# Optimization experiments

Measured on AMD Instinct MI355X. Metric: run time of the kernel, lower is better.

Reference implementation:

```python
import jax, jax.numpy as jnp
import numpy as np

# graph/batch constants
B, N_PER, DEG, FEAT, K = 64, 1024, 16, 64, 10
N = B * N_PER            # 65536 total nodes
E = N * DEG              # 1048576 edges
HID = 2 * FEAT           # 128


def setup_inputs() -> dict:
    key = jax.random.key(0)
    ks = jax.random.split(key, 10)
    x = jax.random.normal(ks[0], (N, FEAT), jnp.float32)
    # intra-graph edges: local indices in [0, n) offset by graph id * n
    offs = (jnp.arange(B, dtype=jnp.int32) * N_PER)[:, None]
    edge_src = (jax.random.randint(ks[1], (B, N_PER * DEG), 0, N_PER, jnp.int32) + offs).reshape(-1)
    edge_dst = (jax.random.randint(ks[2], (B, N_PER * DEG), 0, N_PER, jnp.int32) + offs).reshape(-1)
    uniforms = jax.random.uniform(ks[3], (N, 3 * K), jnp.float32, 1e-6, 1.0 - 1e-6)

    def lin(k, i, o):
        s = 1.0 / np.sqrt(i)
        return jax.random.uniform(k, (i, o), jnp.float32, -s, s)

    return {
        "x": x, "edge_src": edge_src, "edge_dst": edge_dst, "uniforms": uniforms,
        "W0": lin(ks[4], FEAT, HID), "b0": jnp.zeros((HID,), jnp.float32),
        "W1": lin(ks[5], HID, HID), "b1": jnp.zeros((HID,), jnp.float32),
        "Wf": lin(ks[6], HID, HID), "bf": jnp.zeros((HID,), jnp.float32),
        "W2": lin(ks[7], 2 * HID, HID), "b2": jnp.zeros((HID,), jnp.float32),
        "W3": lin(ks[8], HID, 1), "b3": jnp.zeros((1,), jnp.float32),
    }


def _gcn_norm(src, dst):
    # GCNConv: add self-loops, symmetric deg^{-1/2} normalization
    loop = jnp.arange(N, dtype=src.dtype)
    s = jnp.concatenate([src, loop])
    d = jnp.concatenate([dst, loop])
    deg = jnp.zeros((N,), jnp.float32).at[d].add(1.0)
    dinv = jax.lax.rsqrt(deg)  # deg >= 1 because of self-loops
    return s, d, dinv[s] * dinv[d]


def _gcn(h, W, b, s, d, norm):
    h = h @ W                                                   # [N, out]
    agg = jnp.zeros((N, W.shape[1]), h.dtype).at[d].add(h[s] * norm[:, None])
    return agg + b


def reference(x, edge_src, edge_dst, uniforms, W0, b0, W1, b1, Wf, bf, W2, b2, W3, b3):
    s, d, norm = _gcn_norm(edge_src, edge_dst)
    # conv0 + global max pool + fc1 -> per-graph global info
    h0 = jax.nn.relu(_gcn(x, W0, b0, s, d, norm))               # [N, HID]
    glob = jnp.max(h0.reshape(B, N_PER, HID), axis=1) @ Wf + bf  # [B, HID]
    # two applications of the SAME conv1 (as in the source)
    h = jax.nn.relu(_gcn(h0, W1, b1, s, d, norm))
    h = jax.nn.relu(_gcn(h, W1, b1, s, d, norm))
    # ConcatenateLayer: [local, tiled global] per node (dropout is eval identity)
    h = jnp.concatenate([h, jnp.repeat(glob, N_PER, axis=0)], axis=-1)  # [N, 2*HID]
    h = jax.nn.relu(_gcn(h, W2, b2, s, d, norm))
    logits = _gcn(h, W3, b3, s, d, norm).reshape(B, N_PER)      # [B, n]
    # SampleConcrete (eval): per-graph top-k threshold mask
    th = jax.lax.top_k(logits, K)[0][:, -1]                     # kth-largest per graph
    mask = (logits >= th[:, None]).astype(jnp.float32)
    return mask.reshape(N, 1)
```

## Files before the change

### kernel.cpp

```cpp
#include <hip/hip_runtime.h>
#include <math.h>

#define NB    64
#define NPER  1024
#define NTOT  65536
#define ETOT  1048576
#define FEAT  64
#define HID   128
#define KSEL  10
#define MAXDEG 64


typedef __attribute__((ext_vector_type(8))) short bf16x8;
typedef __attribute__((ext_vector_type(4))) float f32x4;

static __device__ __forceinline__ unsigned short f2bf(float x) {
    unsigned u = __float_as_uint(x);
    return (unsigned short)((u + 0x7FFFu + ((u >> 16) & 1u)) >> 16);
}
static __device__ __forceinline__ float bf2f(unsigned short s) {
    return __uint_as_float(((unsigned)s) << 16);
}

__global__ __launch_bounds__(1024) void csrpack_k(const int* __restrict__ src,
                                                  const int* __restrict__ dst,
                                                  int* __restrict__ cnt,
                                                  unsigned short* __restrict__ col16,
                                                  const float* __restrict__ W0,
                                                  const float* __restrict__ W1,
                                                  const float* __restrict__ W2,
                                                  unsigned short* __restrict__ Wph,
                                                  unsigned short* __restrict__ Wpl,
                                                  float* __restrict__ part) {
    int t = threadIdx.x;
    int b = blockIdx.x;
    if (b >= NB) {
        int pb = b - NB;
        if (pb == 40) {
            for (int i = t; i < NB * 128; i += 1024) part[i] = 0.f;
            return;
        }
        int idx = pb * 1024 + t;
        if (idx >= 320 * 128) return;
        int k = idx >> 7;
        int c = idx & 127;
        float v;
        size_t mb;
        int kk;
        if (k < 64)       { kk = k;       v = W0[kk * 128 + c]; mb = 0; }
        else if (k < 192) { kk = k - 64;  v = W1[kk * 128 + c]; mb = (size_t)64 * 128; }
        else              { kk = k - 192; v = W2[kk * 128 + c]; mb = (size_t)192 * 128; }
        unsigned short h  = f2bf(v);
        unsigned short lo = f2bf(v - bf2f(h));
        size_t d = mb + ((size_t)(kk >> 3) * 128 + c) * 8 + (kk & 7);
        Wph[d] = h;
        Wpl[d] = lo;
        return;
    }
    __shared__ int lcnt[NPER];
    int g = b;
    int gbase = g << 10;
    int ebase = g * (NPER * 16);
    lcnt[t] = 0;
    __syncthreads();
    const int* ds = dst + ebase;
    const int* ss = src + ebase;
#pragma unroll 1
    for (int i = 0; i < 16; ++i) {
        int e = i * 1024 + t;
        int d = ds[e] & (NPER - 1);
        int s = ss[e] & (NPER - 1);
        int pos = atomicAdd(&lcnt[d], 1);
        col16[(size_t)pos * NTOT + gbase + d] = (unsigned short)s;
    }
    __syncthreads();
    cnt[gbase + t] = lcnt[t];
}

__global__ __launch_bounds__(1024) void agg_k(const float* __restrict__ Z,
                                              const float* __restrict__ x,
                                              const unsigned short* __restrict__ col16,
                                              const int* __restrict__ cnt,
                                              unsigned short* __restrict__ Ah,
                                              unsigned short* __restrict__ Al,
                                              int cshift,
                                              float* __restrict__ fvec,
                                              const float* __restrict__ Wf,
                                              const float* __restrict__ bfv,
                                              const float* __restrict__ W2g,
                                              float* __restrict__ gproj,
                                              const float* __restrict__ part) {
    __shared__ float4 sy4[4096];
    int t = threadIdx.x;

    if (Wf && (int)blockIdx.x >= (int)gridDim.x - NB) {
        float* sm = (float*)sy4;
        float* mp = sm;
        float* ps = sm + 128;
        float* gl = sm + 128 + 1024;
        int gg = blockIdx.x - (gridDim.x - NB);
        int o = t & 127, s8 = t >> 7;
        if (t < 128) mp[t] = part[(size_t)gg * 128 + t];
        __syncthreads();
        float p = 0.f;
#pragma unroll
        for (int q = 0; q < 16; ++q) { int k = s8 * 16 + q; p += mp[k] * Wf[(size_t)k * 128 + o]; }
        ps[t] = p;
        __syncthreads();
        if (t < 128) {
            float a = bfv[t];
#pragma unroll
            for (int q = 0; q < 8; ++q) a += ps[q * 128 + t];
            gl[t] = a;
        }
        __syncthreads();
        p = 0.f;
#pragma unroll
        for (int q = 0; q < 16; ++q) { int k = s8 * 16 + q; p += gl[k] * W2g[(size_t)(128 + k) * 128 + o]; }
        ps[t] = p;
        __syncthreads();
        if (t < 128) {
            float a = 0.f;
#pragma unroll
            for (int q = 0; q < 8; ++q) a += ps[q * 128 + t];
            gproj[(size_t)gg * 128 + t] = a;
        }
        return;
    }

    int g = blockIdx.x >> cshift;
    int c = blockIdx.x & ((1 << cshift) - 1);
    int gbase = g << 10;

    if (x) {
#pragma unroll
        for (int j = 0; j < 4; ++j) {
            int fl = j * 1024 + t;
            int v = fl >> 2, q = fl & 3;
            float dvv = rsqrtf((float)cnt[gbase + v] + 1.0f);
            float4 z = *(const float4*)&x[(size_t)(gbase + v) * FEAT + c * 16 + q * 4];
            z.x *= dvv; z.y *= dvv; z.z *= dvv; z.w *= dvv;
            sy4[fl] = z;
        }
    } else {
        const float4* Zg4 = (const float4*)(Z + ((size_t)c * NTOT + gbase) * 16);
#pragma unroll
        for (int j = 0; j < 4; ++j) sy4[j * 1024 + t] = Zg4[j * 1024 + t];
    }
    __syncthreads();

    int f4 = t & 3;
    int vl = t >> 2;

#pragma unroll 1
    for (int pass = 0; pass < 4; ++pass) {
        int v = pass * 256 + vl;
        int gv = gbase + v;
        int n = cnt[gv];
        float dv = rsqrtf((float)n + 1.0f);
        const unsigned short* ip = col16 + gv;
        float4 acc = sy4[v * 4 + f4];
        int i = 0;
        for (; i + 4 <= n; i += 4) {
            int a0 = ip[(size_t)(i + 0) * NTOT];
            int a1 = ip[(size_t)(i + 1) * NTOT];
            int a2 = ip[(size_t)(i + 2) * NTOT];
            int a3 = ip[(size_t)(i + 3) * NTOT];
            float4 y0 = sy4[a0 * 4 + f4];
            float4 y1 = sy4[a1 * 4 + f4];
            float4 y2 = sy4[a2 * 4 + f4];
            float4 y3 = sy4[a3 * 4 + f4];
            acc.x += (y0.x + y1.x) + (y2.x + y3.x);
            acc.y += (y0.y + y1.y) + (y2.y + y3.y);
            acc.z += (y0.z + y1.z) + (y2.z + y3.z);
            acc.w += (y0.w + y1.w) + (y2.w + y3.w);
        }
        for (; i < n; ++i) {
            float4 ya = sy4[(int)ip[(size_t)i * NTOT] * 4 + f4];
            acc.x += ya.x; acc.y += ya.y; acc.z += ya.z; acc.w += ya.w;
        }
        acc.x *= dv; acc.y *= dv; acc.z *= dv; acc.w *= dv;
        int krow = c * 16 + f4 * 4;
        size_t ba = ((size_t)(krow >> 3) * NTOT + gv) * 8 + (krow & 7);
        ushort4 h, lo;
        h.x = f2bf(acc.x); lo.x = f2bf(acc.x - bf2f(h.x));
        h.y = f2bf(acc.y); lo.y = f2bf(acc.y - bf2f(h.y));
        h.z = f2bf(acc.z); lo.z = f2bf(acc.z - bf2f(h.z));
        h.w = f2bf(acc.w); lo.w = f2bf(acc.w - bf2f(h.w));
        *(ushort4*)&Ah[ba] = h;
        *(ushort4*)&Al[ba] = lo;
    }

    if (fvec && c == 0) {
        __syncthreads();
        float* sdv = (float*)sy4;
        float dv = rsqrtf((float)cnt[gbase + t] + 1.0f);
        sdv[t] = dv;
        __syncthreads();
        int n = cnt[gbase + t];
        float acc = dv;
        const unsigned short* ip = col16 + gbase + t;
        for (int i = 0; i < n; ++i) acc += sdv[ip[(size_t)i * NTOT]];
        fvec[gbase + t] = dv * acc;
    }
}

__global__ __launch_bounds__(256, 4) void gemm_k(const unsigned short* __restrict__ Ah,
                                                 const unsigned short* __restrict__ Al,
                                                 const unsigned short* __restrict__ Wph,
                                                 const unsigned short* __restrict__ Wpl,
                                                 const float* __restrict__ bias,
                                                 float* __restrict__ outZ,
                                                 int K,
                                                 const float* __restrict__ fvec,
                                                 const float* __restrict__ gproj,
                                                 float* __restrict__ part,
                                                 const float* __restrict__ W3,
                                                 const int* __restrict__ cnt,
                                                 float* __restrict__ zout) {
    __shared__ __align__(16) unsigned short sAh[64 * 128];
    __shared__ __align__(16) unsigned short sAl[64 * 128];
    __shared__ float zred[4 * 64];

    int t = threadIdx.x;
    int row0 = blockIdx.x * 64;
    int w = t >> 6;
    int l = t & 63;
    int lr = l & 15;
    int hg = l >> 4;

    f32x4 acc[4][2];
#pragma unroll
    for (int m = 0; m < 4; ++m)
#pragma unroll
        for (int n = 0; n < 2; ++n) acc[m][n] = (f32x4){0.f, 0.f, 0.f, 0.f};

    int nu = (K >> 3) << 6 >> 8;
    for (int i = 0; i < nu; ++i) {
        int u = t + i * 256;
        int p = u >> 6, r = u & 63;
        size_t src = ((size_t)p * NTOT + row0 + r) * 8;
        *(uint4*)&sAh[u * 8] = *(const uint4*)&Ah[src];
        *(uint4*)&sAl[u * 8] = *(const uint4*)&Al[src];
    }
    __syncthreads();

    int nk = K >> 5;
#pragma unroll 1
    for (int s = 0; s < nk; ++s) {
        int pb = s * 4 + hg;
        bf16x8 ah[4], al[4], bh[2], bl[2];
#pragma unroll
        for (int m = 0; m < 4; ++m) {
            ah[m] = *(const bf16x8*)&sAh[(pb * 64 + m * 16 + lr) * 8];
            al[m] = *(const bf16x8*)&sAl[(pb * 64 + m * 16 + lr) * 8];
        }
#pragma unroll
        for (int n = 0; n < 2; ++n) {
            size_t wb = ((size_t)pb * 128 + w * 32 + n * 16 + lr) * 8;
            bh[n] = *(const bf16x8*)&Wph[wb];
            bl[n] = *(const bf16x8*)&Wpl[wb];
        }
#pragma unroll
        for (int m = 0; m < 4; ++m)
#pragma unroll
            for (int n = 0; n < 2; ++n) {
                acc[m][n] = __builtin_amdgcn_mfma_f32_16x16x32_bf16(ah[m], bh[n], acc[m][n], 0, 0, 0);
                acc[m][n] = __builtin_amdgcn_mfma_f32_16x16x32_bf16(al[m], bh[n], acc[m][n], 0, 0, 0);
                acc[m][n] = __builtin_amdgcn_mfma_f32_16x16x32_bf16(ah[m], bl[n], acc[m][n], 0, 0, 0);
            }
    }

    int g = row0 >> 10;
    int wc0 = w * 32;
    float bb[2], gp[2], w3c[2];
#pragma unroll
    for (int n = 0; n < 2; ++n) {
        int col = wc0 + n * 16 + lr;
        bb[n]  = bias[col];
        gp[n]  = fvec ? gproj[(size_t)g * 128 + col] : 0.f;
        w3c[n] = zout ? W3[col] : 0.f;
    }
    float fr[4][4];
    if (fvec) {
#pragma unroll
        for (int m = 0; m < 4; ++m)
#pragma unroll
            for (int r = 0; r < 4; ++r) fr[m][r] = fvec[row0 + m * 16 + hg * 4 + r];
    }
    float dvs[4][4];
    if (outZ) {
#pragma unroll
        for (int m = 0; m < 4; ++m)
#pragma unroll
            for (int r = 0; r < 4; ++r)
                dvs[m][r] = rsqrtf((float)cnt[row0 + m * 16 + hg * 4 + r] + 1.0f);
    }
    float zp[4][4];
#pragma unroll
    for (int m = 0; m < 4; ++m)
#pragma unroll
        for (int r = 0; r < 4; ++r) zp[m][r] = 0.f;
    float cmx[2] = {0.f, 0.f};

#pragma unroll
    for (int m = 0; m < 4; ++m)
#pragma unroll
        for (int n = 0; n < 2; ++n)
#pragma unroll
            for (int r = 0; r < 4; ++r) {
                float v = acc[m][n][r] + bb[n];
                if (fvec) v += fr[m][r] * gp[n];
                v = fmaxf(v, 0.f);
                if (part) cmx[n] = fmaxf(cmx[n], v);
                if (zout) zp[m][r] += v * w3c[n];
                if (outZ) {
                    int row = row0 + m * 16 + hg * 4 + r;
                    int cidx = w * 2 + n;
                    outZ[((size_t)cidx * NTOT + row) * 16 + lr] = v * dvs[m][r];
                }
            }

    if (part) {
#pragma unroll
        for (int n = 0; n < 2; ++n) {
            float v = cmx[n];
            v = fmaxf(v, __shfl_xor(v, 16));
            v = fmaxf(v, __shfl_xor(v, 32));
            if (hg == 0)
                atomicMax((int*)&part[(size_t)g * 128 + wc0 + n * 16 + lr],
                          __float_as_int(v));
        }
    }

    if (zout) {
#pragma unroll
        for (int m = 0; m < 4; ++m)
#pragma unroll
            for (int r = 0; r < 4; ++r) {
                float v = zp[m][r];
                v += __shfl_xor(v, 1);
                v += __shfl_xor(v, 2);
                v += __shfl_xor(v, 4);
                v += __shfl_xor(v, 8);
                zp[m][r] = v;
            }
        if (lr == 0) {
#pragma unroll
            for (int m = 0; m < 4; ++m)
#pragma unroll
                for (int r = 0; r < 4; ++r)
                    zred[w * 64 + m * 16 + hg * 4 + r] = zp[m][r];
        }
        __syncthreads();
        if (t < 64) {
            float sZ = zred[t] + zred[64 + t] + zred[128 + t] + zred[192 + t];
            zout[row0 + t] = sZ * rsqrtf((float)cnt[row0 + t] + 1.0f);
        }
    }
}

__global__ __launch_bounds__(1024) void smask_k(const float* __restrict__ z,
                                                const unsigned short* __restrict__ col16,
                                                const int* __restrict__ cnt,
                                                const float* __restrict__ b3,
                                                float* __restrict__ out) {
    __shared__ float sz[1024];
    __shared__ float sl[1024];
    __shared__ float slo[1024];
    __shared__ float rv[16];
    __shared__ int   ri[16];
    __shared__ float sth;
    int g = blockIdx.x, t = threadIdx.x;
    int wv = t >> 6, ln = t & 63;
    int base = g << 10;
    sz[t] = z[base + t];
    __syncthreads();
    float bb = b3[0];
    {
        int gv = base + t;
        int n = cnt[gv];
        float dv = rsqrtf((float)n + 1.0f);
        float acc = sz[t];
        const unsigned short* ip = col16 + gv;
        int j = 0;
        for (; j + 2 <= n; j += 2)
            acc += sz[ip[(size_t)j * NTOT]] + sz[ip[(size_t)(j + 1) * NTOT]];
        for (; j < n; ++j) acc += sz[ip[(size_t)j * NTOT]];
        float lg = acc * dv + bb;
        sl[t] = lg; slo[t] = lg;
    }
    __syncthreads();
    for (int pass = 0; pass < KSEL; ++pass) {
        float bv = sl[t];
        int bi = t;
#pragma unroll
        for (int off = 32; off; off >>= 1) {
            float ov = __shfl_xor(bv, off);
            int   oi = __shfl_xor(bi, off);
            if (ov > bv || (ov == bv && oi < bi)) { bv = ov; bi = oi; }
        }
        if (ln == 0) { rv[wv] = bv; ri[wv] = bi; }
        __syncthreads();
        if (t == 0) {
            float mv = rv[0]; int mi = ri[0];
#pragma unroll
            for (int q = 1; q < 16; ++q)
                if (rv[q] > mv || (rv[q] == mv && ri[q] < mi)) { mv = rv[q]; mi = ri[q]; }
            sth = mv; sl[mi] = -INFINITY;
        }
        __syncthreads();
    }
    float th = sth;
    out[base + t] = (slo[t] >= th) ? 1.f : 0.f;
}

extern "C" void kernel_launch(void* const* d_in, const int* in_sizes, int n_in,
                              void* d_out, int out_size, void* d_ws, size_t ws_size,
                              hipStream_t stream) {
    const float* x        = (const float*)d_in[0];
    const int*   edge_src = (const int*)d_in[1];
    const int*   edge_dst = (const int*)d_in[2];
    const float* W0 = (const float*)d_in[4];
    const float* b0 = (const float*)d_in[5];
    const float* W1 = (const float*)d_in[6];
    const float* b1 = (const float*)d_in[7];
    const float* Wf = (const float*)d_in[8];
    const float* bf = (const float*)d_in[9];
    const float* W2 = (const float*)d_in[10];
    const float* b2 = (const float*)d_in[11];
    const float* W3 = (const float*)d_in[12];
    const float* b3 = (const float*)d_in[13];
    float* out = (float*)d_out;

    char* w = (char*)d_ws;
    int*            cnt   = (int*)w;            w += (size_t)NTOT * 4;
    unsigned short* col16 = (unsigned short*)w; w += (size_t)NTOT * MAXDEG * 2;
    float*          fvec  = (float*)w;          w += (size_t)NTOT * 4;
    unsigned short* Ah    = (unsigned short*)w; w += (size_t)NTOT * 128 * 2;
    unsigned short* Al    = (unsigned short*)w; w += (size_t)NTOT * 128 * 2;
    float*          Q     = (float*)w;          w += (size_t)NTOT * 128 * 4;
    float*          part  = (float*)w;          w += (size_t)NB * 128 * 4;
    float*          gproj = (float*)w;          w += (size_t)NB * 128 * 4;
    float*          z     = (float*)w;          w += (size_t)NTOT * 4;
    unsigned short* Wph   = (unsigned short*)w; w += (size_t)320 * 128 * 2;
    unsigned short* Wpl   = (unsigned short*)w; w += (size_t)320 * 128 * 2;

    csrpack_k<<<NB + 41, 1024, 0, stream>>>(edge_src, edge_dst, cnt, col16,
                                            W0, W1, W2, Wph, Wpl, part);

    agg_k<<<NB * 4, 1024, 0, stream>>>(nullptr, x, col16, cnt, Ah, Al, 2, nullptr,
                                       nullptr, nullptr, nullptr, nullptr, nullptr);
    gemm_k<<<NTOT / 64, 256, 0, stream>>>(Ah, Al, Wph, Wpl, b0, Q, FEAT,
                                          nullptr, nullptr, part, nullptr, cnt, nullptr);

    agg_k<<<NB * 8 + NB, 1024, 0, stream>>>(Q, nullptr, col16, cnt, Ah, Al, 3, nullptr,
                                            Wf, bf, W2, gproj, part);
    gemm_k<<<NTOT / 64, 256, 0, stream>>>(Ah, Al, Wph + 64 * 128, Wpl + 64 * 128, b1, Q,
                                          HID, nullptr, nullptr, nullptr, nullptr, cnt,
                                          nullptr);
    agg_k<<<NB * 8, 1024, 0, stream>>>(Q, nullptr, col16, cnt, Ah, Al, 3, nullptr,
                                       nullptr, nullptr, nullptr, nullptr, nullptr);
    gemm_k<<<NTOT / 64, 256, 0, stream>>>(Ah, Al, Wph + 64 * 128, Wpl + 64 * 128, b1, Q,
                                          HID, nullptr, nullptr, nullptr, nullptr, cnt,
                                          nullptr);

    agg_k<<<NB * 8, 1024, 0, stream>>>(Q, nullptr, col16, cnt, Ah, Al, 3, fvec,
                                       nullptr, nullptr, nullptr, nullptr, nullptr);
    gemm_k<<<NTOT / 64, 256, 0, stream>>>(Ah, Al, Wph + 192 * 128, Wpl + 192 * 128, b2,
                                          nullptr, HID, fvec, gproj, nullptr, W3, cnt, z);

    smask_k<<<NB, 1024, 0, stream>>>(z, col16, cnt, b3, out);
}
```

Measured before the change: 289.6 us.

## Switch neighbor list to row-major per-node layout with vectorized index loads

Changes the padded adjacency storage from slot-major (slot*NTOT+node) to node-major (node*MAXDEG+slot), so each node's neighbor indices sit together. The aggregation, degree-vector and final logit kernels then read four indices per ushort4 load instead of four strided scalar loads, and the CSR packing kernel reads edges as int4. The aim is fewer memory transactions per neighbor index. The trade-off is that adjacent threads now read indices 128 bytes apart, which loses coalescing across lanes. The scatter writes in the pack kernel also become more scattered.

```diff
diff --git a/kernel.cpp b/kernel.cpp
--- a/kernel.cpp
+++ b/kernel.cpp
@@ -63,15 +63,25 @@
     int ebase = g * (NPER * 16);
     lcnt[t] = 0;
     __syncthreads();
-    const int* ds = dst + ebase;
-    const int* ss = src + ebase;
+    const int4* ds4 = (const int4*)(dst + ebase);
+    const int4* ss4 = (const int4*)(src + ebase);
 #pragma unroll 1
-    for (int i = 0; i < 16; ++i) {
-        int e = i * 1024 + t;
-        int d = ds[e] & (NPER - 1);
-        int s = ss[e] & (NPER - 1);
-        int pos = atomicAdd(&lcnt[d], 1);
-        col16[(size_t)pos * NTOT + gbase + d] = (unsigned short)s;
+    for (int i = 0; i < 4; ++i) {
+        int e4 = i * 1024 + t;
+        int4 dv = ds4[e4];
+        int4 sv = ss4[e4];
+        int d0 = dv.x & (NPER - 1), s0 = sv.x & (NPER - 1);
+        int d1 = dv.y & (NPER - 1), s1 = sv.y & (NPER - 1);
+        int d2 = dv.z & (NPER - 1), s2 = sv.z & (NPER - 1);
+        int d3 = dv.w & (NPER - 1), s3 = sv.w & (NPER - 1);
+        int p0 = atomicAdd(&lcnt[d0], 1);
+        col16[(size_t)(gbase + d0) * MAXDEG + p0] = (unsigned short)s0;
+        int p1 = atomicAdd(&lcnt[d1], 1);
+        col16[(size_t)(gbase + d1) * MAXDEG + p1] = (unsigned short)s1;
+        int p2 = atomicAdd(&lcnt[d2], 1);
+        col16[(size_t)(gbase + d2) * MAXDEG + p2] = (unsigned short)s2;
+        int p3 = atomicAdd(&lcnt[d3], 1);
+        col16[(size_t)(gbase + d3) * MAXDEG + p3] = (unsigned short)s3;
     }
     __syncthreads();
     cnt[gbase + t] = lcnt[t];
@@ -158,25 +168,22 @@
         int gv = gbase + v;
         int n = cnt[gv];
         float dv = rsqrtf((float)n + 1.0f);
-        const unsigned short* ip = col16 + gv;
+        const unsigned short* ip = col16 + (size_t)gv * MAXDEG;
         float4 acc = sy4[v * 4 + f4];
         int i = 0;
         for (; i + 4 <= n; i += 4) {
-            int a0 = ip[(size_t)(i + 0) * NTOT];
-            int a1 = ip[(size_t)(i + 1) * NTOT];
-            int a2 = ip[(size_t)(i + 2) * NTOT];
-            int a3 = ip[(size_t)(i + 3) * NTOT];
-            float4 y0 = sy4[a0 * 4 + f4];
-            float4 y1 = sy4[a1 * 4 + f4];
-            float4 y2 = sy4[a2 * 4 + f4];
-            float4 y3 = sy4[a3 * 4 + f4];
+            ushort4 s4 = *(const ushort4*)&ip[i];
+            float4 y0 = sy4[(int)s4.x * 4 + f4];
+            float4 y1 = sy4[(int)s4.y * 4 + f4];
+            float4 y2 = sy4[(int)s4.z * 4 + f4];
+            float4 y3 = sy4[(int)s4.w * 4 + f4];
             acc.x += (y0.x + y1.x) + (y2.x + y3.x);
             acc.y += (y0.y + y1.y) + (y2.y + y3.y);
             acc.z += (y0.z + y1.z) + (y2.z + y3.z);
             acc.w += (y0.w + y1.w) + (y2.w + y3.w);
         }
         for (; i < n; ++i) {
-            float4 ya = sy4[(int)ip[(size_t)i * NTOT] * 4 + f4];
+            float4 ya = sy4[(int)ip[i] * 4 + f4];
             acc.x += ya.x; acc.y += ya.y; acc.z += ya.z; acc.w += ya.w;
         }
         acc.x *= dv; acc.y *= dv; acc.z *= dv; acc.w *= dv;
@@ -199,8 +206,13 @@
         __syncthreads();
         int n = cnt[gbase + t];
         float acc = dv;
-        const unsigned short* ip = col16 + gbase + t;
-        for (int i = 0; i < n; ++i) acc += sdv[ip[(size_t)i * NTOT]];
+        const unsigned short* ip = col16 + (size_t)(gbase + t) * MAXDEG;
+        int i = 0;
+        for (; i + 4 <= n; i += 4) {
+            ushort4 s4 = *(const ushort4*)&ip[i];
+            acc += (sdv[s4.x] + sdv[s4.y]) + (sdv[s4.z] + sdv[s4.w]);
+        }
+        for (; i < n; ++i) acc += sdv[ip[i]];
         fvec[gbase + t] = dv * acc;
     }
 }
@@ -382,11 +394,13 @@
         int n = cnt[gv];
         float dv = rsqrtf((float)n + 1.0f);
         float acc = sz[t];
-        const unsigned short* ip = col16 + gv;
+        const unsigned short* ip = col16 + (size_t)gv * MAXDEG;
         int j = 0;
-        for (; j + 2 <= n; j += 2)
-            acc += sz[ip[(size_t)j * NTOT]] + sz[ip[(size_t)(j + 1) * NTOT]];
-        for (; j < n; ++j) acc += sz[ip[(size_t)j * NTOT]];
+        for (; j + 4 <= n; j += 4) {
+            ushort4 s4 = *(const ushort4*)&ip[j];
+            acc += (sz[s4.x] + sz[s4.y]) + (sz[s4.z] + sz[s4.w]);
+        }
+        for (; j < n; ++j) acc += sz[ip[j]];
         float lg = acc * dv + bb;
         sl[t] = lg; slo[t] = lg;
     }
```

Result: slower. 299.4 us (+3.4%).
